# Kernel tuning notes

Hardware: AMD Instinct MI355X
Metric: run time of the kernel (lower is better)

The kernel has to match this reference:

```python
import jax, jax.numpy as jnp
import numpy as np

K = 3  # number of nearest neighbors for interpolation
BIG = 1e10  # masks out cross-batch pairs in the distance matrix


def setup_inputs() -> dict:
    key = jax.random.key(0)
    ks = jax.random.split(key, 8)
    N, Ns, C, Cs, B = 4096, 16384, 256, 128, 4
    Din, H = C + Cs, 256
    return {
        "x": jax.random.normal(ks[0], (N, C), dtype=jnp.float32),
        "pos": jax.random.normal(ks[1], (N, 3), dtype=jnp.float32),
        "batch": jnp.sort(jax.random.randint(ks[2], (N,), 0, B)),
        "x_skip": jax.random.normal(ks[3], (Ns, Cs), dtype=jnp.float32),
        "pos_skip": jax.random.normal(ks[4], (Ns, 3), dtype=jnp.float32),
        "batch_skip": jnp.sort(jax.random.randint(ks[5], (Ns,), 0, B)),
        "W1": jax.random.normal(ks[6], (Din, H), dtype=jnp.float32) * (1.0 / np.sqrt(Din)),
        "b1": jnp.zeros((H,), dtype=jnp.float32),
        "W2": jax.random.normal(ks[7], (H, H), dtype=jnp.float32) * (1.0 / np.sqrt(H)),
        "b2": jnp.zeros((H,), dtype=jnp.float32),
    }


def reference(x, pos, batch, x_skip, pos_skip, batch_skip, W1, b1, W2, b2):
    # knn_interpolate: squared distances from each fine point to all coarse points,
    # masked so neighbors only come from the same batch element.
    d2 = jnp.sum((pos_skip[:, None, :] - pos[None, :, :]) ** 2, axis=-1)  # [Ns, N]
    d2 = jnp.where(batch_skip[:, None] != batch[None, :], BIG, d2)
    neg_d2, idx = jax.lax.top_k(-d2, K)          # k smallest distances, [Ns, K]
    w = 1.0 / jnp.clip(-neg_d2, 1e-16)           # inverse-squared-distance weights
    num = jnp.sum(x[idx] * w[..., None], axis=1)  # [Ns, C] weighted gather-reduce
    y = num / jnp.sum(w, axis=1, keepdims=True)
    # concat skip features, then MLP (Linear-ReLU-Linear-ReLU)
    y = jnp.concatenate([y, x_skip], axis=1)      # [Ns, C + Cs]
    h = jax.nn.relu(y @ W1 + b1)
    out = jax.nn.relu(h @ W2 + b2)
    return (out, pos_skip, batch_skip)
```

## Files before the change

### kernel.cpp

```cpp
#include <hip/hip_runtime.h>
#include <stdint.h>

#define NPTS   4096
#define NSKIP  16384
#define CCH    256
#define CSK    128
#define DIN    384
#define HDIM   256
#define BIGF   1e10f

typedef unsigned short u16;
typedef __attribute__((ext_vector_type(8))) short short8;
typedef __attribute__((ext_vector_type(4))) float floatx4;

__device__ __forceinline__ u16 f2bf(float f) {
    union { float f; uint32_t u; } c; c.f = f;
    uint32_t u = c.u;
    return (u16)((u + 0x7FFFu + ((u >> 16) & 1u)) >> 16);
}

__device__ __forceinline__ double pkkey(float d, int j) {
    return __hiloint2double(__float_as_int(d), j);
}

__global__ __launch_bounds__(256) void prep_kernel(
    const float* __restrict__ W1, const float* __restrict__ W2,
    u16* __restrict__ W1p, u16* __restrict__ W2p,
    const float* __restrict__ pos, float4* __restrict__ pos4,
    const int* __restrict__ batch, int* __restrict__ range)
{
    const int bid = blockIdx.x;
    const int t = threadIdx.x;

    const float* W = (bid < 48) ? W1 : W2;
    u16* Wp       = (bid < 48) ? W1p : W2p;
    const int KT  = (bid < 48) ? 12 : 8;
    const int g   = ((bid < 48) ? bid : (bid - 48)) * 256 + t;

    const int lane = g & 63;
    const int kt = (g >> 6) % KT;
    const int nt = (g >> 6) / KT;
    const int kbase = kt * 32 + (lane >> 4) * 8;
    const int n = nt * 16 + (lane & 15);
    u16 v[8];
#pragma unroll
    for (int j = 0; j < 8; ++j) v[j] = f2bf(W[(size_t)(kbase + j) * HDIM + n]);
#pragma unroll
    for (int j = 0; j < 8; ++j) Wp[(size_t)g * 8 + j] = v[j];

    if (bid >= 48 && bid < 64) {
        const int p = (bid - 48) * 256 + t;
        pos4[p] = make_float4(pos[p * 3 + 0], pos[p * 3 + 1], pos[p * 3 + 2], 0.0f);
    }

    if (bid == 0) {
        for (int j = t * 16; j < t * 16 + 16; ++j) {
            if (j == 0) {
                const int b0 = batch[0];
                for (int b = 0; b <= b0; ++b) range[b] = 0;
            } else {
                const int bp = batch[j - 1], bj = batch[j];
                for (int b = bp + 1; b <= bj; ++b) range[b] = j;
            }
            if (j == NPTS - 1) {
                const int bl = batch[NPTS - 1];
                for (int b = bl + 1; b <= 4; ++b) range[b] = NPTS;
            }
        }
    }
}

__global__ __launch_bounds__(1024, 8) void mega_kernel(
    const float* __restrict__ x, const float* __restrict__ x_skip,
    const float4* __restrict__ pos4, const int* __restrict__ range,
    const u16* __restrict__ W1p, const float* __restrict__ b1,
    const u16* __restrict__ W2p, const float* __restrict__ b2,
    const float* __restrict__ pos_skip, const int* __restrict__ batch_skip,
    float* __restrict__ out)
{
    __shared__ u16 sA[32 * 392];
    __shared__ float sOut[32 * 256];
    const int t = threadIdx.x;
    const int row0 = blockIdx.x * 32;
    const int wave = t >> 6, lane = t & 63;
    const int quad = lane >> 4, ml = lane & 15;
    const int rl = t >> 5;
    const int sub = t & 31;
    const int i = row0 + rl;

    const float4 vs = *(const float4*)(x_skip + (size_t)i * CSK + sub * 4);
    const int b = batch_skip[i];
    const int start = range[b], end = range[b + 1];
    const float px = pos_skip[i * 3 + 0];
    const float py = pos_skip[i * 3 + 1];
    const float pz = pos_skip[i * 3 + 2];
    {
        uint2 pk;
        pk.x = (uint32_t)f2bf(vs.x) | ((uint32_t)f2bf(vs.y) << 16);
        pk.y = (uint32_t)f2bf(vs.z) | ((uint32_t)f2bf(vs.w) << 16);
        *(uint2*)(sA + rl * 392 + CCH + sub * 4) = pk;
    }

    const double BIGKEY = pkkey(BIGF, 0x7FFFFFFF);
    double k0 = BIGKEY, k1 = BIGKEY, k2 = BIGKEY;
    for (int j = start + sub; j < end; j += 32) {
        const float4 q = pos4[j];
        const float dx = __fsub_rn(px, q.x);
        const float dy = __fsub_rn(py, q.y);
        const float dz = __fsub_rn(pz, q.z);
        const float dd = __fadd_rn(__fadd_rn(__fmul_rn(dx, dx), __fmul_rn(dy, dy)),
                                   __fmul_rn(dz, dz));
        const double kk = pkkey(dd, j);
        const double u0 = fmax(k0, kk); k0 = fmin(k0, kk);
        const double u1 = fmax(k1, u0); k1 = fmin(k1, u0);
        k2 = fmin(k2, u1);
    }
#pragma unroll
    for (int m = 1; m < 32; m <<= 1) {
        const double o0 = __shfl_xor(k0, m);
        const double o1 = __shfl_xor(k1, m);
        const double o2 = __shfl_xor(k2, m);
        double u0 = fmax(k0, o0); k0 = fmin(k0, o0);
        double u1 = fmax(k1, u0); k1 = fmin(k1, u0);
        k2 = fmin(k2, u1);
        u1 = fmax(k1, o1); k1 = fmin(k1, o1);
        k2 = fmin(k2, u1);
        k2 = fmin(k2, o2);
    }

    const int i0 = __double2loint(k0);
    const int i1 = __double2loint(k1);
    const int i2 = __double2loint(k2);
    {
        const float d0 = __int_as_float(__double2hiint(k0));
        const float d1 = __int_as_float(__double2hiint(k1));
        const float d2 = __int_as_float(__double2hiint(k2));
        const float w0r = 1.0f / fmaxf(d0, 1e-16f);
        const float w1r = 1.0f / fmaxf(d1, 1e-16f);
        const float w2r = 1.0f / fmaxf(d2, 1e-16f);
        const float inv = 1.0f / (w0r + w1r + w2r);
        const float w0 = w0r * inv, w1 = w1r * inv, w2 = w2r * inv;

        const float* xr0 = x + (size_t)i0 * CCH + sub * 8;
        const float* xr1 = x + (size_t)i1 * CCH + sub * 8;
        const float* xr2 = x + (size_t)i2 * CCH + sub * 8;
        const float4 a0 = *(const float4*)(xr0);
        const float4 a1 = *(const float4*)(xr0 + 4);
        const float4 c0 = *(const float4*)(xr1);
        const float4 c1 = *(const float4*)(xr1 + 4);
        const float4 e0 = *(const float4*)(xr2);
        const float4 e1 = *(const float4*)(xr2 + 4);

        const float y0 = w0 * a0.x + w1 * c0.x + w2 * e0.x;
        const float y1 = w0 * a0.y + w1 * c0.y + w2 * e0.y;
        const float y2 = w0 * a0.z + w1 * c0.z + w2 * e0.z;
        const float y3 = w0 * a0.w + w1 * c0.w + w2 * e0.w;
        const float y4 = w0 * a1.x + w1 * c1.x + w2 * e1.x;
        const float y5 = w0 * a1.y + w1 * c1.y + w2 * e1.y;
        const float y6 = w0 * a1.z + w1 * c1.z + w2 * e1.z;
        const float y7 = w0 * a1.w + w1 * c1.w + w2 * e1.w;
        uint4 pk;
        pk.x = (uint32_t)f2bf(y0) | ((uint32_t)f2bf(y1) << 16);
        pk.y = (uint32_t)f2bf(y2) | ((uint32_t)f2bf(y3) << 16);
        pk.z = (uint32_t)f2bf(y4) | ((uint32_t)f2bf(y5) << 16);
        pk.w = (uint32_t)f2bf(y6) | ((uint32_t)f2bf(y7) << 16);
        *(uint4*)(sA + rl * 392 + sub * 8) = pk;
    }
    __syncthreads();

    floatx4 acc[2] = {};
    {
        const u16* aA = sA + ml * 392 + quad * 8;
        for (int kt = 0; kt < 12; ++kt) {
            short8 a0 = *(const short8*)(aA + kt * 32);
            short8 a1 = *(const short8*)(aA + 16 * 392 + kt * 32);
            short8 bfr = *(const short8*)(W1p + (size_t)((wave * 12 + kt) * 64 + lane) * 8);
            acc[0] = __builtin_amdgcn_mfma_f32_16x16x32_bf16(a0, bfr, acc[0], 0, 0, 0);
            acc[1] = __builtin_amdgcn_mfma_f32_16x16x32_bf16(a1, bfr, acc[1], 0, 0, 0);
        }
    }
    __syncthreads();

    {
        const int n = wave * 16 + ml;
        const float bv = b1[n];
#pragma unroll
        for (int mt = 0; mt < 2; ++mt) {
#pragma unroll
            for (int r = 0; r < 4; ++r) {
                const int m = mt * 16 + quad * 4 + r;
                sA[m * 264 + n] = f2bf(fmaxf(acc[mt][r] + bv, 0.0f));
            }
        }
    }
    __syncthreads();

    floatx4 acc2[2] = {};
    {
        const u16* aH = sA + ml * 264 + quad * 8;
        for (int kt = 0; kt < 8; ++kt) {
            short8 a0 = *(const short8*)(aH + kt * 32);
            short8 a1 = *(const short8*)(aH + 16 * 264 + kt * 32);
            short8 bfr = *(const short8*)(W2p + (size_t)((wave * 8 + kt) * 64 + lane) * 8);
            acc2[0] = __builtin_amdgcn_mfma_f32_16x16x32_bf16(a0, bfr, acc2[0], 0, 0, 0);
            acc2[1] = __builtin_amdgcn_mfma_f32_16x16x32_bf16(a1, bfr, acc2[1], 0, 0, 0);
        }
    }

    {
        const int n = wave * 16 + ml;
        const float bv = b2[n];
#pragma unroll
        for (int mt = 0; mt < 2; ++mt) {
#pragma unroll
            for (int r = 0; r < 4; ++r) {
                const int m = mt * 16 + quad * 4 + r;
                sOut[m * 256 + n] = fmaxf(acc2[mt][r] + bv, 0.0f);
            }
        }
    }
    __syncthreads();
    {
        float* dst = out + (size_t)row0 * HDIM;
#pragma unroll
        for (int k = 0; k < 2; ++k) {
            const int e = t + 1024 * k;
            *(float4*)(dst + e * 4) = *(const float4*)(sOut + e * 4);
        }
    }

    if (t < 128) {
        const int e = blockIdx.x * 128 + t;
        const size_t base = (size_t)NSKIP * HDIM;
        if (e < NSKIP * 3) out[base + e] = pos_skip[e];
        else               out[base + e] = (float)batch_skip[e - NSKIP * 3];
    }
}

extern "C" void kernel_launch(void* const* d_in, const int* in_sizes, int n_in,
                              void* d_out, int out_size, void* d_ws, size_t ws_size,
                              hipStream_t stream) {
    const float* x         = (const float*)d_in[0];
    const float* pos       = (const float*)d_in[1];
    const int*   batch     = (const int*)d_in[2];
    const float* x_skip    = (const float*)d_in[3];
    const float* pos_skip  = (const float*)d_in[4];
    const int*   batch_skip= (const int*)d_in[5];
    const float* W1        = (const float*)d_in[6];
    const float* b1        = (const float*)d_in[7];
    const float* W2        = (const float*)d_in[8];
    const float* b2        = (const float*)d_in[9];
    float* out = (float*)d_out;

    char* ws = (char*)d_ws;
    u16*    W1p   = (u16*)ws;
    u16*    W2p   = (u16*)(ws + 196608);
    int*    range = (int*)(ws + 327680);
    float4* pos4  = (float4*)(ws + 327712);

    prep_kernel<<<80, 256, 0, stream>>>(W1, W2, W1p, W2p, pos, pos4, batch, range);
    mega_kernel<<<NSKIP / 32, 1024, 0, stream>>>(x, x_skip, pos4, range,
                                                 W1p, b1, W2p, b2,
                                                 pos_skip, batch_skip, out);
}
```

Before: 109.0 us.

## Overlap second-half KNN search with first-half MLP MFMA inside each block

Splits each block's 32 rows into two halves. All 16 waves first do the KNN search for rows 0-15, one wave and 64 lanes per row. Waves 0-7 then run the layer-1 and layer-2 MFMAs for those rows while waves 8-15 do KNN for rows 16-31, and the two wave groups stay staggered through the MLP stages. The aim is to hide the latency-bound KNN scan behind matrix-core work within a block. The cost is more divergent wave-specialised code and more barrier stages, and the gain may be small because other resident blocks already overlap the two kinds of work.

Result: slower. 115.6 us (+6.1%).

```diff
diff --git a/kernel.cpp b/kernel.cpp
--- a/kernel.cpp
+++ b/kernel.cpp
@@ -84,54 +84,53 @@
     const int row0 = blockIdx.x * 32;
     const int wave = t >> 6, lane = t & 63;
     const int quad = lane >> 4, ml = lane & 15;
-    const int rl = t >> 5;
-    const int sub = t & 31;
-    const int i = row0 + rl;
-
-    const float4 vs = *(const float4*)(x_skip + (size_t)i * CSK + sub * 4);
-    const int b = batch_skip[i];
-    const int start = range[b], end = range[b + 1];
-    const float px = pos_skip[i * 3 + 0];
-    const float py = pos_skip[i * 3 + 1];
-    const float pz = pos_skip[i * 3 + 2];
+    const double BIGKEY = pkkey(BIGF, 0x7FFFFFFF);
+
     {
+        const int rl = t >> 5, sub = t & 31;
+        const float4 vs = *(const float4*)(x_skip + (size_t)(row0 + rl) * CSK + sub * 4);
         uint2 pk;
         pk.x = (uint32_t)f2bf(vs.x) | ((uint32_t)f2bf(vs.y) << 16);
         pk.y = (uint32_t)f2bf(vs.z) | ((uint32_t)f2bf(vs.w) << 16);
         *(uint2*)(sA + rl * 392 + CCH + sub * 4) = pk;
     }
-
-    const double BIGKEY = pkkey(BIGF, 0x7FFFFFFF);
-    double k0 = BIGKEY, k1 = BIGKEY, k2 = BIGKEY;
-    for (int j = start + sub; j < end; j += 32) {
-        const float4 q = pos4[j];
-        const float dx = __fsub_rn(px, q.x);
-        const float dy = __fsub_rn(py, q.y);
-        const float dz = __fsub_rn(pz, q.z);
-        const float dd = __fadd_rn(__fadd_rn(__fmul_rn(dx, dx), __fmul_rn(dy, dy)),
-                                   __fmul_rn(dz, dz));
-        const double kk = pkkey(dd, j);
-        const double u0 = fmax(k0, kk); k0 = fmin(k0, kk);
-        const double u1 = fmax(k1, u0); k1 = fmin(k1, u0);
-        k2 = fmin(k2, u1);
-    }
-#pragma unroll
-    for (int m = 1; m < 32; m <<= 1) {
-        const double o0 = __shfl_xor(k0, m);
-        const double o1 = __shfl_xor(k1, m);
-        const double o2 = __shfl_xor(k2, m);
-        double u0 = fmax(k0, o0); k0 = fmin(k0, o0);
-        double u1 = fmax(k1, u0); k1 = fmin(k1, u0);
-        k2 = fmin(k2, u1);
-        u1 = fmax(k1, o1); k1 = fmin(k1, o1);
-        k2 = fmin(k2, u1);
-        k2 = fmin(k2, o2);
-    }
-
-    const int i0 = __double2loint(k0);
-    const int i1 = __double2loint(k1);
-    const int i2 = __double2loint(k2);
     {
+        const int rl = wave;
+        const int i = row0 + rl;
+        const int b = batch_skip[i];
+        const int start = range[b], end = range[b + 1];
+        const float px = pos_skip[i * 3 + 0];
+        const float py = pos_skip[i * 3 + 1];
+        const float pz = pos_skip[i * 3 + 2];
+
+        double k0 = BIGKEY, k1 = BIGKEY, k2 = BIGKEY;
+        for (int j = start + lane; j < end; j += 64) {
+            const float4 q = pos4[j];
+            const float dx = __fsub_rn(px, q.x);
+            const float dy = __fsub_rn(py, q.y);
+            const float dz = __fsub_rn(pz, q.z);
+            const float dd = __fadd_rn(__fadd_rn(__fmul_rn(dx, dx), __fmul_rn(dy, dy)),
+                                       __fmul_rn(dz, dz));
+            const double kk = pkkey(dd, j);
+            const double u0 = fmax(k0, kk); k0 = fmin(k0, kk);
+            const double u1 = fmax(k1, u0); k1 = fmin(k1, u0);
+            k2 = fmin(k2, u1);
+        }
+#pragma unroll
+        for (int m = 1; m < 64; m <<= 1) {
+            const double o0 = __shfl_xor(k0, m);
+            const double o1 = __shfl_xor(k1, m);
+            const double o2 = __shfl_xor(k2, m);
+            double u0 = fmax(k0, o0); k0 = fmin(k0, o0);
+            double u1 = fmax(k1, u0); k1 = fmin(k1, u0);
+            k2 = fmin(k2, u1);
+            u1 = fmax(k1, o1); k1 = fmin(k1, o1);
+            k2 = fmin(k2, u1);
+            k2 = fmin(k2, o2);
+        }
+        const int i0 = __double2loint(k0);
+        const int i1 = __double2loint(k1);
+        const int i2 = __double2loint(k2);
         const float d0 = __int_as_float(__double2hiint(k0));
         const float d1 = __int_as_float(__double2hiint(k1));
         const float d2 = __int_as_float(__double2hiint(k2));
@@ -140,7 +139,78 @@
         const float w2r = 1.0f / fmaxf(d2, 1e-16f);
         const float inv = 1.0f / (w0r + w1r + w2r);
         const float w0 = w0r * inv, w1 = w1r * inv, w2 = w2r * inv;
-
+        const float4 a = *(const float4*)(x + (size_t)i0 * CCH + lane * 4);
+        const float4 c = *(const float4*)(x + (size_t)i1 * CCH + lane * 4);
+        const float4 e = *(const float4*)(x + (size_t)i2 * CCH + lane * 4);
+        const float y0 = w0 * a.x + w1 * c.x + w2 * e.x;
+        const float y1 = w0 * a.y + w1 * c.y + w2 * e.y;
+        const float y2 = w0 * a.z + w1 * c.z + w2 * e.z;
+        const float y3 = w0 * a.w + w1 * c.w + w2 * e.w;
+        uint2 pk;
+        pk.x = (uint32_t)f2bf(y0) | ((uint32_t)f2bf(y1) << 16);
+        pk.y = (uint32_t)f2bf(y2) | ((uint32_t)f2bf(y3) << 16);
+        *(uint2*)(sA + rl * 392 + lane * 4) = pk;
+    }
+    __syncthreads();
+
+    floatx4 acc[2] = {};
+    if (wave < 8) {
+        const u16* aA = sA + ml * 392 + quad * 8;
+        for (int kt = 0; kt < 12; ++kt) {
+            short8 a0 = *(const short8*)(aA + kt * 32);
+#pragma unroll
+            for (int nt = 0; nt < 2; ++nt) {
+                const int ntile = 2 * wave + nt;
+                short8 bfr = *(const short8*)(W1p + (size_t)((ntile * 12 + kt) * 64 + lane) * 8);
+                acc[nt] = __builtin_amdgcn_mfma_f32_16x16x32_bf16(a0, bfr, acc[nt], 0, 0, 0);
+            }
+        }
+    } else {
+        const int rl = 16 + ((wave - 8) << 1) + (lane >> 5);
+        const int sub = lane & 31;
+        const int i = row0 + rl;
+        const int b = batch_skip[i];
+        const int start = range[b], end = range[b + 1];
+        const float px = pos_skip[i * 3 + 0];
+        const float py = pos_skip[i * 3 + 1];
+        const float pz = pos_skip[i * 3 + 2];
+
+        double k0 = BIGKEY, k1 = BIGKEY, k2 = BIGKEY;
+        for (int j = start + sub; j < end; j += 32) {
+            const float4 q = pos4[j];
+            const float dx = __fsub_rn(px, q.x);
+            const float dy = __fsub_rn(py, q.y);
+            const float dz = __fsub_rn(pz, q.z);
+            const float dd = __fadd_rn(__fadd_rn(__fmul_rn(dx, dx), __fmul_rn(dy, dy)),
+                                       __fmul_rn(dz, dz));
+            const double kk = pkkey(dd, j);
+            const double u0 = fmax(k0, kk); k0 = fmin(k0, kk);
+            const double u1 = fmax(k1, u0); k1 = fmin(k1, u0);
+            k2 = fmin(k2, u1);
+        }
+#pragma unroll
+        for (int m = 1; m < 32; m <<= 1) {
+            const double o0 = __shfl_xor(k0, m);
+            const double o1 = __shfl_xor(k1, m);
+            const double o2 = __shfl_xor(k2, m);
+            double u0 = fmax(k0, o0); k0 = fmin(k0, o0);
+            double u1 = fmax(k1, u0); k1 = fmin(k1, u0);
+            k2 = fmin(k2, u1);
+            u1 = fmax(k1, o1); k1 = fmin(k1, o1);
+            k2 = fmin(k2, u1);
+            k2 = fmin(k2, o2);
+        }
+        const int i0 = __double2loint(k0);
+        const int i1 = __double2loint(k1);
+        const int i2 = __double2loint(k2);
+        const float d0 = __int_as_float(__double2hiint(k0));
+        const float d1 = __int_as_float(__double2hiint(k1));
+        const float d2 = __int_as_float(__double2hiint(k2));
+        const float w0r = 1.0f / fmaxf(d0, 1e-16f);
+        const float w1r = 1.0f / fmaxf(d1, 1e-16f);
+        const float w2r = 1.0f / fmaxf(d2, 1e-16f);
+        const float inv = 1.0f / (w0r + w1r + w2r);
+        const float w0 = w0r * inv, w1 = w1r * inv, w2 = w2r * inv;
         const float* xr0 = x + (size_t)i0 * CCH + sub * 8;
         const float* xr1 = x + (size_t)i1 * CCH + sub * 8;
         const float* xr2 = x + (size_t)i2 * CCH + sub * 8;
@@ -150,7 +220,6 @@
         const float4 c1 = *(const float4*)(xr1 + 4);
         const float4 e0 = *(const float4*)(xr2);
         const float4 e1 = *(const float4*)(xr2 + 4);
-
         const float y0 = w0 * a0.x + w1 * c0.x + w2 * e0.x;
         const float y1 = w0 * a0.y + w1 * c0.y + w2 * e0.y;
         const float y2 = w0 * a0.z + w1 * c0.z + w2 * e0.z;
@@ -168,58 +237,92 @@
     }
     __syncthreads();
 
-    floatx4 acc[2] = {};
-    {
-        const u16* aA = sA + ml * 392 + quad * 8;
+    if (wave >= 8) {
+        const u16* aA = sA + (16 + ml) * 392 + quad * 8;
         for (int kt = 0; kt < 12; ++kt) {
-            short8 a0 = *(const short8*)(aA + kt * 32);
-            short8 a1 = *(const short8*)(aA + 16 * 392 + kt * 32);
-            short8 bfr = *(const short8*)(W1p + (size_t)((wave * 12 + kt) * 64 + lane) * 8);
-            acc[0] = __builtin_amdgcn_mfma_f32_16x16x32_bf16(a0, bfr, acc[0], 0, 0, 0);
-            acc[1] = __builtin_amdgcn_mfma_f32_16x16x32_bf16(a1, bfr, acc[1], 0, 0, 0);
-        }
-    }
-    __syncthreads();
-
-    {
-        const int n = wave * 16 + ml;
-        const float bv = b1[n];
-#pragma unroll
-        for (int mt = 0; mt < 2; ++mt) {
+            short8 a1 = *(const short8*)(aA + kt * 32);
+#pragma unroll
+            for (int nt = 0; nt < 2; ++nt) {
+                const int ntile = 2 * (wave - 8) + nt;
+                short8 bfr = *(const short8*)(W1p + (size_t)((ntile * 12 + kt) * 64 + lane) * 8);
+                acc[nt] = __builtin_amdgcn_mfma_f32_16x16x32_bf16(a1, bfr, acc[nt], 0, 0, 0);
+            }
+        }
+    } else {
+#pragma unroll
+        for (int nt = 0; nt < 2; ++nt) {
+            const int n = (2 * wave + nt) * 16 + ml;
+            const float bv = b1[n];
 #pragma unroll
             for (int r = 0; r < 4; ++r) {
-                const int m = mt * 16 + quad * 4 + r;
-                sA[m * 264 + n] = f2bf(fmaxf(acc[mt][r] + bv, 0.0f));
+                const int m = quad * 4 + r;
+                sA[m * 264 + n] = f2bf(fmaxf(acc[nt][r] + bv, 0.0f));
             }
         }
     }
     __syncthreads();
 
     floatx4 acc2[2] = {};
-    {
+    if (wave < 8) {
         const u16* aH = sA + ml * 264 + quad * 8;
         for (int kt = 0; kt < 8; ++kt) {
             short8 a0 = *(const short8*)(aH + kt * 32);
-            short8 a1 = *(const short8*)(aH + 16 * 264 + kt * 32);
-            short8 bfr = *(const short8*)(W2p + (size_t)((wave * 8 + kt) * 64 + lane) * 8);
-            acc2[0] = __builtin_amdgcn_mfma_f32_16x16x32_bf16(a0, bfr, acc2[0], 0, 0, 0);
-            acc2[1] = __builtin_amdgcn_mfma_f32_16x16x32_bf16(a1, bfr, acc2[1], 0, 0, 0);
-        }
-    }
-
-    {
-        const int n = wave * 16 + ml;
-        const float bv = b2[n];
-#pragma unroll
-        for (int mt = 0; mt < 2; ++mt) {
+#pragma unroll
+            for (int nt = 0; nt < 2; ++nt) {
+                const int ntile = 2 * wave + nt;
+                short8 bfr = *(const short8*)(W2p + (size_t)((ntile * 8 + kt) * 64 + lane) * 8);
+                acc2[nt] = __builtin_amdgcn_mfma_f32_16x16x32_bf16(a0, bfr, acc2[nt], 0, 0, 0);
+            }
+        }
+    } else {
+#pragma unroll
+        for (int nt = 0; nt < 2; ++nt) {
+            const int n = (2 * (wave - 8) + nt) * 16 + ml;
+            const float bv = b1[n];
 #pragma unroll
             for (int r = 0; r < 4; ++r) {
-                const int m = mt * 16 + quad * 4 + r;
-                sOut[m * 256 + n] = fmaxf(acc2[mt][r] + bv, 0.0f);
-            }
-        }
-    }
-    __syncthreads();
+                const int m = 16 + quad * 4 + r;
+                sA[m * 264 + n] = f2bf(fmaxf(acc[nt][r] + bv, 0.0f));
+            }
+        }
+    }
+    __syncthreads();
+
+    if (wave >= 8) {
+        const u16* aH = sA + (16 + ml) * 264 + quad * 8;
+        for (int kt = 0; kt < 8; ++kt) {
+            short8 a1 = *(const short8*)(aH + kt * 32);
+#pragma unroll
+            for (int nt = 0; nt < 2; ++nt) {
+                const int ntile = 2 * (wave - 8) + nt;
+                short8 bfr = *(const short8*)(W2p + (size_t)((ntile * 8 + kt) * 64 + lane) * 8);
+                acc2[nt] = __builtin_amdgcn_mfma_f32_16x16x32_bf16(a1, bfr, acc2[nt], 0, 0, 0);
+            }
+        }
+#pragma unroll
+        for (int nt = 0; nt < 2; ++nt) {
+            const int n = (2 * (wave - 8) + nt) * 16 + ml;
+            const float bv = b2[n];
+#pragma unroll
+            for (int r = 0; r < 4; ++r) {
+                const int m = 16 + quad * 4 + r;
+                sOut[m * 256 + n] = fmaxf(acc2[nt][r] + bv, 0.0f);
+            }
+        }
+    } else {
+#pragma unroll
+        for (int nt = 0; nt < 2; ++nt) {
+            const int n = (2 * wave + nt) * 16 + ml;
+            const float bv = b2[n];
+#pragma unroll
+            for (int r = 0; r < 4; ++r) {
+                const int m = quad * 4 + r;
+                sOut[m * 256 + n] = fmaxf(acc2[nt][r] + bv, 0.0f);
+            }
+        }
+    }
+    __syncthreads();
+
     {
         float* dst = out + (size_t)row0 * HDIM;
 #pragma unroll
@@ -228,7 +331,6 @@
             *(float4*)(dst + e * 4) = *(const float4*)(sOut + e * 4);
         }
     }
-
     if (t < 128) {
         const int e = blockIdx.x * 128 + t;
         const size_t base = (size_t)NSKIP * HDIM;
```
